# Kernel tuning notes

Measured on AMD Instinct MI355X. Metric: run time of the kernel, lower is better.

## Reference

```python
import jax, jax.numpy as jnp
import numpy as np

B, T, C = 2, 2048, 2048
N_HEADS, N_KV_HEADS = 16, 4
HEAD_DIM = C // N_HEADS  # 128
NUM_GROUPS = N_HEADS // N_KV_HEADS  # 4


def setup_inputs() -> dict:
    key = jax.random.key(0)
    ks = jax.random.split(key, 5)
    s = 1.0 / np.sqrt(C)
    return {
        "x": jax.random.normal(ks[0], (B, T, C), dtype=jnp.float32),
        "Wq": jax.random.normal(ks[1], (C, N_HEADS * HEAD_DIM), dtype=jnp.float32) * s,
        "Wk": jax.random.normal(ks[2], (C, N_KV_HEADS * HEAD_DIM), dtype=jnp.float32) * s,
        "Wv": jax.random.normal(ks[3], (C, N_KV_HEADS * HEAD_DIM), dtype=jnp.float32) * s,
        "Wo": jax.random.normal(ks[4], (C, C), dtype=jnp.float32) * s,
    }


def _rope_tables(seq_len, head_dim, dtype):
    theta = 1.0 / (10000.0 ** (jnp.arange(0, head_dim, 2, dtype=jnp.float32) / head_dim))
    freqs = jnp.arange(seq_len, dtype=jnp.float32)[:, None] * theta[None, :]  # [T, hd/2]
    cos = jnp.concatenate([jnp.cos(freqs), jnp.cos(freqs)], axis=-1)  # [T, hd]
    sin = jnp.concatenate([jnp.sin(freqs), jnp.sin(freqs)], axis=-1)
    return cos.astype(dtype), sin.astype(dtype)


def _rotate_half(x):
    x1, x2 = jnp.split(x, 2, axis=-1)
    return jnp.concatenate([-x2, x1], axis=-1)


def reference(x, Wq, Wk, Wv, Wo):
    b, t, c = x.shape
    q = (x @ Wq).reshape(b, t, N_HEADS, HEAD_DIM).transpose(0, 2, 1, 3)      # [B,H,T,hd]
    k = (x @ Wk).reshape(b, t, N_KV_HEADS, HEAD_DIM).transpose(0, 2, 1, 3)   # [B,Hkv,T,hd]
    v = (x @ Wv).reshape(b, t, N_KV_HEADS, HEAD_DIM).transpose(0, 2, 1, 3)

    cos, sin = _rope_tables(t, HEAD_DIM, x.dtype)  # [T,hd]
    cos = cos[None, None]  # [1,1,T,hd]
    sin = sin[None, None]
    q = q * cos + _rotate_half(q) * sin
    k = k * cos + _rotate_half(k) * sin

    # GQA: expand kv heads (repeat_interleave along head dim)
    k = jnp.repeat(k, NUM_GROUPS, axis=1)  # [B,H,T,hd]
    v = jnp.repeat(v, NUM_GROUPS, axis=1)

    scale = 1.0 / jnp.sqrt(jnp.asarray(HEAD_DIM, dtype=x.dtype))
    scores = jnp.einsum("bhqd,bhkd->bhqk", q, k) * scale  # [B,H,T,T]
    causal = jnp.tril(jnp.ones((t, t), dtype=bool))
    scores = jnp.where(causal[None, None], scores, jnp.asarray(-jnp.inf, dtype=scores.dtype))
    attn = jax.nn.softmax(scores, axis=-1)
    out = jnp.einsum("bhqk,bhkd->bhqd", attn, v)  # [B,H,T,hd]
    out = out.transpose(0, 2, 1, 3).reshape(b, t, c)
    return out @ Wo
```

## Files before the change

kernel.cpp:

```cpp
#include <hip/hip_runtime.h>
#include <hip/hip_bf16.h>
#include <math.h>

typedef __hip_bfloat16 bf16;
typedef __attribute__((ext_vector_type(8))) short bf16x8;
typedef __attribute__((ext_vector_type(4))) float floatx4;

__device__ __forceinline__ void async_copy16(const bf16* g, bf16* l) {
    __builtin_amdgcn_global_load_lds(
        (__attribute__((address_space(1))) void*)(void*)g,
        (__attribute__((address_space(3))) void*)(void*)l,
        16, 0, 0);
}

__global__ __launch_bounds__(256) void cast_f32_bf16(const float* __restrict__ in,
                                                     bf16* __restrict__ out, int n4) {
    int i = blockIdx.x * 256 + threadIdx.x;
    if (i >= n4) return;
    float4 v = ((const float4*)in)[i];
    union { ushort4 u; bf16 b[4]; } o;
    o.b[0] = __float2bfloat16(v.x);
    o.b[1] = __float2bfloat16(v.y);
    o.b[2] = __float2bfloat16(v.z);
    o.b[3] = __float2bfloat16(v.w);
    ((ushort4*)out)[i] = o.u;
}

__global__ __launch_bounds__(256) void cast_transpose(const float* __restrict__ in,
                                                      bf16* __restrict__ out, int K, int N) {
    __shared__ float tile[32][33];
    int nb = blockIdx.x * 32, kb = blockIdx.y * 32;
    for (int j = threadIdx.y; j < 32; j += 8)
        tile[j][threadIdx.x] = in[(size_t)(kb + j) * N + nb + threadIdx.x];
    __syncthreads();
    for (int j = threadIdx.y; j < 32; j += 8)
        out[(size_t)(nb + j) * K + kb + threadIdx.x] = __float2bfloat16(tile[threadIdx.x][j]);
}

template <bool OUTF32>
__global__ __launch_bounds__(256) void gemm_bt(const bf16* __restrict__ A,
                                               const bf16* __restrict__ Bt,
                                               void* __restrict__ Cout,
                                               int M, int N, int K) {
    __shared__ bf16 As[128 * 32];
    __shared__ bf16 Bs[128 * 32];
    const int tid = threadIdx.x;
    const int wave = tid >> 6, lane = tid & 63;
    const int c = lane & 15, quad = lane >> 4;
    const int wm = wave >> 1, wn = wave & 1;
    const int mBase = blockIdx.y * 128, nBase = blockIdx.x * 128;

    const int sRow = lane >> 2;
    const int sCol = ((lane & 3) ^ ((lane >> 3) & 3)) << 3;
    const int rdOff = (quad ^ ((c >> 1) & 3)) << 3;
    const bf16* gA = A + (size_t)(mBase + wave * 32 + sRow) * K + sCol;
    const bf16* gB = Bt + (size_t)(nBase + wave * 32 + sRow) * K + sCol;
    bf16* lA = As + wave * 1024;
    bf16* lB = Bs + wave * 1024;

    floatx4 acc[4][4];
#pragma unroll
    for (int mt = 0; mt < 4; mt++)
#pragma unroll
        for (int nt = 0; nt < 4; nt++) acc[mt][nt] = (floatx4){0.f, 0.f, 0.f, 0.f};

    for (int k0 = 0; k0 < K; k0 += 32) {
        async_copy16(gA + k0, lA);
        async_copy16(gA + k0 + 16 * K, lA + 512);
        async_copy16(gB + k0, lB);
        async_copy16(gB + k0 + 16 * K, lB + 512);
        __syncthreads();
        bf16x8 af[4], bfr[4];
#pragma unroll
        for (int mt = 0; mt < 4; mt++)
            af[mt] = *(const bf16x8*)(As + (wm * 64 + mt * 16 + c) * 32 + rdOff);
#pragma unroll
        for (int nt = 0; nt < 4; nt++)
            bfr[nt] = *(const bf16x8*)(Bs + (wn * 64 + nt * 16 + c) * 32 + rdOff);
#pragma unroll
        for (int mt = 0; mt < 4; mt++)
#pragma unroll
            for (int nt = 0; nt < 4; nt++)
                acc[mt][nt] = __builtin_amdgcn_mfma_f32_16x16x32_bf16(af[mt], bfr[nt],
                                                                      acc[mt][nt], 0, 0, 0);
        __syncthreads();
    }
#pragma unroll
    for (int mt = 0; mt < 4; mt++)
#pragma unroll
        for (int nt = 0; nt < 4; nt++)
#pragma unroll
            for (int r = 0; r < 4; r++) {
                int row = mBase + wm * 64 + mt * 16 + quad * 4 + r;
                int col = nBase + wn * 64 + nt * 16 + c;
                if (OUTF32)
                    ((float*)Cout)[(size_t)row * N + col] = acc[mt][nt][r];
                else
                    ((bf16*)Cout)[(size_t)row * N + col] = __float2bfloat16(acc[mt][nt][r]);
            }
}

__global__ __launch_bounds__(512) void gemm256(const bf16* __restrict__ A,
                                               const bf16* __restrict__ Bt,
                                               bf16* __restrict__ C,
                                               int M, int N, int K) {
    __shared__ bf16 As[4][256 * 32];
    __shared__ bf16 Bs[4][256 * 32];
    const int tid = threadIdx.x;
    const int wave = tid >> 6, lane = tid & 63;
    const int c = lane & 15, quad = lane >> 4;
    const int wm = wave >> 2, wn = wave & 3;
    const int mBase = blockIdx.y * 256, nBase = blockIdx.x * 256;
    const int rdOff = (quad ^ ((c >> 1) & 3)) << 3;

    const bf16* gAs[2];
    const bf16* gBs[2];
#pragma unroll
    for (int i = 0; i < 2; i++) {
        int ci = i * 512 + tid;
        int r = ci >> 2;
        int sc = (ci & 3) ^ ((r >> 1) & 3);
        gAs[i] = A + (size_t)(mBase + r) * K + sc * 8;
        gBs[i] = Bt + (size_t)(nBase + r) * K + sc * 8;
    }
    const int ldsW = wave * 512;

    floatx4 acc[8][4];
#pragma unroll
    for (int mt = 0; mt < 8; mt++)
#pragma unroll
        for (int nt = 0; nt < 4; nt++) acc[mt][nt] = (floatx4){0.f, 0.f, 0.f, 0.f};

    auto stage_half = [&](int t, int i) {
        const int bb = t & 3;
        const int lo = i * 4096 + ldsW;
        async_copy16(gAs[i] + (size_t)t * 32, &As[bb][0] + lo);
        async_copy16(gBs[i] + (size_t)t * 32, &Bs[bb][0] + lo);
    };

    auto tile_body = [&](int t, bool doStage) {
        const int bb = t & 3;
        const bf16* as = &As[bb][0];
        const bf16* bs = &Bs[bb][0];
        bf16x8 bfr[4], af[4];
#pragma unroll
        for (int nt = 0; nt < 4; nt++)
            bfr[nt] = *(const bf16x8*)(bs + (wn * 64 + nt * 16 + c) * 32 + rdOff);
#pragma unroll
        for (int mt = 0; mt < 4; mt++)
            af[mt] = *(const bf16x8*)(as + (wm * 128 + mt * 16 + c) * 32 + rdOff);
        if (doStage) stage_half(t + 2, 0);
        __builtin_amdgcn_s_setprio(1);
#pragma unroll
        for (int mt = 0; mt < 4; mt++)
#pragma unroll
            for (int nt = 0; nt < 4; nt++)
                acc[mt][nt] = __builtin_amdgcn_mfma_f32_16x16x32_bf16(af[mt], bfr[nt],
                                                                      acc[mt][nt], 0, 0, 0);
        __builtin_amdgcn_s_setprio(0);
#pragma unroll
        for (int mt = 0; mt < 4; mt++)
            af[mt] = *(const bf16x8*)(as + (wm * 128 + 64 + mt * 16 + c) * 32 + rdOff);
        if (doStage) stage_half(t + 2, 1);
        __builtin_amdgcn_s_setprio(1);
#pragma unroll
        for (int mt = 0; mt < 4; mt++)
#pragma unroll
            for (int nt = 0; nt < 4; nt++)
                acc[4 + mt][nt] = __builtin_amdgcn_mfma_f32_16x16x32_bf16(af[mt], bfr[nt],
                                                                          acc[4 + mt][nt], 0, 0, 0);
        __builtin_amdgcn_s_setprio(0);
    };

    const int NT = K >> 5;
    stage_half(0, 0); stage_half(0, 1);
    stage_half(1, 0); stage_half(1, 1);
    asm volatile("s_waitcnt vmcnt(4)\n\ts_barrier" ::: "memory");

    for (int t = 0; t < NT - 2; ++t) {
        tile_body(t, true);
        asm volatile("s_waitcnt vmcnt(4)\n\ts_barrier" ::: "memory");
    }
    tile_body(NT - 2, false);
    asm volatile("s_waitcnt vmcnt(0)\n\ts_barrier" ::: "memory");
    tile_body(NT - 1, false);

#pragma unroll
    for (int mt = 0; mt < 8; mt++)
#pragma unroll
        for (int nt = 0; nt < 4; nt++)
#pragma unroll
            for (int r = 0; r < 4; r++) {
                int row = mBase + wm * 128 + mt * 16 + quad * 4 + r;
                int col = nBase + wn * 64 + nt * 16 + c;
                C[(size_t)row * N + col] = __float2bfloat16(acc[mt][nt][r]);
            }
}

__global__ __launch_bounds__(256) void rope_kernel(bf16* __restrict__ X, int heads, int rowStride) {
    int idx = blockIdx.x * 256 + threadIdx.x;
    int d = idx & 63;
    int h = (idx >> 6) % heads;
    int row = idx / (heads * 64);
    int t = row & 2047;
    float theta = exp2f(-(float)d * 0.20762050593045827f);
    float ang = (float)t * theta;
    float sv, cv;
    __sincosf(ang, &sv, &cv);
    bf16* p = X + (size_t)row * rowStride + h * 128 + d;
    float x1 = __bfloat162float(p[0]);
    float x2 = __bfloat162float(p[64]);
    p[0]  = __float2bfloat16(x1 * cv - x2 * sv);
    p[64] = __float2bfloat16(x2 * cv + x1 * sv);
}

__global__ __launch_bounds__(256) void vtrans(const bf16* __restrict__ QKV,
                                              bf16* __restrict__ Vtg) {
    __shared__ bf16 tile[32][34];
    const int bh = blockIdx.z;
    const int b = bh >> 2, kvh = bh & 3;
    const int t0 = blockIdx.x * 32, d0 = blockIdx.y * 32;
    const bf16* src = QKV + (size_t)b * 2048 * 3072 + 2560 + kvh * 128;
    const int tx = threadIdx.x;
    for (int j = threadIdx.y; j < 32; j += 8)
        tile[j][tx] = src[(size_t)(t0 + j) * 3072 + d0 + tx];
    __syncthreads();
    bf16* dst = Vtg + (size_t)bh * 128 * 2048;
    const int g = tx >> 2;
    const int txp = (((g & 3) << 1) | (g >> 2)) * 4 + (tx & 3);
    for (int j = threadIdx.y; j < 32; j += 8)
        dst[(size_t)(d0 + j) * 2048 + t0 + txp] = tile[tx][j];
}

__global__ __launch_bounds__(256, 4) void flash_attn5(const bf16* __restrict__ QKV,
                                                      const bf16* __restrict__ Vtg,
                                                      bf16* __restrict__ Slot0,
                                                      bf16* __restrict__ Slot1,
                                                      float* __restrict__ Ls) {
    const int T = 2048, STR = 3072;
    __shared__ bf16 Ks[4 * 64 * 32];
    __shared__ bf16 Vs[2 * 128 * 32];
    const int b = blockIdx.z, h = blockIdx.y;
    const int pj = blockIdx.x >> 1, s = blockIdx.x & 1;
    const int kvh = h >> 2;
    const int tid = threadIdx.x, wave = tid >> 6, lane = tid & 63;
    const int c = lane & 15, quad = lane >> 4;
    const float C2 = 0.12751541717525597f;

    const bf16* Kg = QKV + (size_t)b * T * STR + 2048 + kvh * 128;
    const bf16* Vg = Vtg + (size_t)(b * 4 + kvh) * 128 * 2048;
    const int srow = tid >> 2;
    const int xcol = ((tid & 3) ^ ((tid >> 3) & 3)) << 3;
    const int koff = (quad ^ ((c >> 1) & 3)) << 3;
    const int qa = 31 - pj;

    auto run_part = [&](int qtile, int ktlo, int kthi, bf16* slot, int lsSlot) {
        const int q0 = qtile * 64;
        bf16x8 qf[4];
        {
            const bf16* qp = QKV + ((size_t)b * T + q0 + wave * 16 + c) * STR + h * 128 + quad * 8;
#pragma unroll
            for (int ks = 0; ks < 4; ks++) qf[ks] = *(const bf16x8*)(qp + ks * 32);
            const float t = (float)(q0 + wave * 16 + c);
#pragma unroll
            for (int ks = 0; ks < 2; ks++)
#pragma unroll
                for (int j = 0; j < 8; j++) {
                    int d = ks * 32 + quad * 8 + j;
                    float theta = exp2f((float)d * -0.20762050593045827f);
                    float sv, cv;
                    __sincosf(t * theta, &sv, &cv);
                    float lo = __bfloat162float(((const bf16*)&qf[ks])[j]);
                    float hi = __bfloat162float(((const bf16*)&qf[ks + 2])[j]);
                    ((bf16*)&qf[ks])[j]     = __float2bfloat16((lo * cv - hi * sv) * C2);
                    ((bf16*)&qf[ks + 2])[j] = __float2bfloat16((hi * cv + lo * sv) * C2);
                }
        }
        floatx4 accO[8];
#pragma unroll
        for (int nt = 0; nt < 8; nt++) accO[nt] = (floatx4){0.f, 0.f, 0.f, 0.f};
        float lsum = 0.f;

        for (int kt = ktlo; kt < kthi; kt++) {
            const int kt0 = kt * 64;
#pragma unroll
            for (int it = 0; it < 4; it++) {
                async_copy16(Kg + (size_t)(kt0 + srow) * STR + it * 32 + xcol,
                             Ks + it * 2048 + wave * 512);
                async_copy16(Vg + (size_t)((it & 1) * 64 + srow) * 2048 + kt0 + (it >> 1) * 32 + xcol,
                             Vs + it * 2048 + wave * 512);
            }
            __syncthreads();
            floatx4 sf[4];
#pragma unroll
            for (int nt = 0; nt < 4; nt++) sf[nt] = (floatx4){0.f, 0.f, 0.f, 0.f};
#pragma unroll
            for (int ks = 0; ks < 4; ks++)
#pragma unroll
                for (int nt = 0; nt < 4; nt++) {
                    bf16x8 kf = *(const bf16x8*)(Ks + ks * 2048 + (nt * 16 + c) * 32 + koff);
                    sf[nt] = __builtin_amdgcn_mfma_f32_16x16x32_bf16(kf, qf[ks], sf[nt], 0, 0, 0);
                }
            if (kt == qtile) {
                const int qrel = wave * 16 + c;
#pragma unroll
                for (int nt = 0; nt < 4; nt++)
#pragma unroll
                    for (int r = 0; r < 4; r++) {
                        float p = exp2f(sf[nt][r]);
                        if (nt * 16 + quad * 4 + r > qrel) p = 0.f;
                        lsum += p;
                        sf[nt][r] = p;
                    }
            } else {
#pragma unroll
                for (int nt = 0; nt < 4; nt++)
#pragma unroll
                    for (int r = 0; r < 4; r++) {
                        float p = exp2f(sf[nt][r]);
                        lsum += p;
                        sf[nt][r] = p;
                    }
            }
#pragma unroll
            for (int kc = 0; kc < 2; kc++) {
                bf16x8 pf;
#pragma unroll
                for (int j = 0; j < 4; j++) {
                    ((bf16*)&pf)[j]     = __float2bfloat16(sf[2 * kc][j]);
                    ((bf16*)&pf)[4 + j] = __float2bfloat16(sf[2 * kc + 1][j]);
                }
#pragma unroll
                for (int nt = 0; nt < 8; nt++) {
                    bf16x8 vf = *(const bf16x8*)(Vs + kc * 4096 + (nt * 16 + c) * 32 + koff);
                    accO[nt] = __builtin_amdgcn_mfma_f32_16x16x32_bf16(pf, vf, accO[nt], 0, 0, 0);
                }
            }
            __syncthreads();
        }
        {
            float v = lsum;
            v += __shfl_xor(v, 16);
            v += __shfl_xor(v, 32);
            if (quad == 0)
                Ls[(size_t)lsSlot * 65536 + ((size_t)(b * 16 + h) * 32 + qtile) * 64
                   + wave * 16 + c] = v;
        }
        const size_t orow = (size_t)b * T + q0 + wave * 16 + quad * 4;
#pragma unroll
        for (int nt = 0; nt < 8; nt++)
#pragma unroll
            for (int r = 0; r < 4; r++)
                slot[(orow + r) * 2048 + h * 128 + nt * 16 + c] =
                    __float2bfloat16(accO[nt][r]);
    };

    if (s == 0) {
        run_part(qa, 0, 17, Slot0, 0);
    } else {
        run_part(qa, 17, 32 - pj, Slot1, 1);
        run_part(pj, 0, pj + 1, Slot0, 0);
    }
}

__global__ __launch_bounds__(256) void attn_merge(bf16* __restrict__ AO,
                                                  const bf16* __restrict__ P1,
                                                  const float* __restrict__ Ls) {
    int i = blockIdx.x * 256 + threadIdx.x;
    int row = i >> 8;
    int cg = (i & 255) << 3;
    int b = row >> 11, t = row & 2047;
    int qtile = t >> 6;
    int h = cg >> 7;
    size_t off = (size_t)row * 2048 + cg;
    size_t li = ((size_t)(b * 16 + h) * 32 + qtile) * 64 + (t & 63);
    bf16x8 a0 = *(const bf16x8*)(AO + off);
    float l = Ls[li];
    float acc[8];
#pragma unroll
    for (int j = 0; j < 8; j++) acc[j] = __bfloat162float(((const bf16*)&a0)[j]);
    if (qtile >= 16) {
        bf16x8 a1 = *(const bf16x8*)(P1 + off);
        l += Ls[65536 + li];
#pragma unroll
        for (int j = 0; j < 8; j++) acc[j] += __bfloat162float(((const bf16*)&a1)[j]);
    }
    float inv = 1.0f / l;
    bf16x8 o;
#pragma unroll
    for (int j = 0; j < 8; j++) ((bf16*)&o)[j] = __float2bfloat16(acc[j] * inv);
    *(bf16x8*)(AO + off) = o;
}

extern "C" void kernel_launch(void* const* d_in, const int* in_sizes, int n_in,
                              void* d_out, int out_size, void* d_ws, size_t ws_size,
                              hipStream_t stream) {
    const float* x  = (const float*)d_in[0];
    const float* Wq = (const float*)d_in[1];
    const float* Wk = (const float*)d_in[2];
    const float* Wv = (const float*)d_in[3];
    const float* Wo = (const float*)d_in[4];

    char* ws = (char*)d_ws;
    bf16* xb   = (bf16*)(ws);
    bf16* Vtg  = (bf16*)(ws);
    bf16* Slt1 = (bf16*)(ws + 4194304);
    float* Ls  = (float*)(ws + 20971520);
    bf16* Wt   = (bf16*)(ws + 16777216);
    bf16* Wot  = (bf16*)(ws + 29360128);
    bf16* QKV  = (bf16*)(ws + 37748736);
    bf16* AO   = (bf16*)(ws + 62914560);

    cast_f32_bf16<<<8192, 256, 0, stream>>>(x, xb, 2097152);
    cast_transpose<<<dim3(64, 64), dim3(32, 8), 0, stream>>>(Wq, Wt, 2048, 2048);
    cast_transpose<<<dim3(16, 64), dim3(32, 8), 0, stream>>>(Wk, Wt + 2048 * 2048, 2048, 512);
    cast_transpose<<<dim3(16, 64), dim3(32, 8), 0, stream>>>(Wv, Wt + 2560 * 2048, 2048, 512);
    cast_transpose<<<dim3(64, 64), dim3(32, 8), 0, stream>>>(Wo, Wot, 2048, 2048);

    gemm256<<<dim3(12, 16), 512, 0, stream>>>(xb, Wt, QKV, 4096, 3072, 2048);

    rope_kernel<<<4096, 256, 0, stream>>>(QKV + 2048, 4, 3072);

    vtrans<<<dim3(64, 4, 8), dim3(32, 8), 0, stream>>>(QKV, Vtg);

    flash_attn5<<<dim3(32, 16, 2), 256, 0, stream>>>(QKV, Vtg, AO, Slt1, Ls);

    attn_merge<<<4096, 256, 0, stream>>>(AO, Slt1, Ls);

    gemm_bt<true><<<dim3(16, 32), 256, 0, stream>>>(AO, Wot, d_out, 4096, 2048, 2048);
}
```

Baseline: 309.4 us.

## Generalize pipelined 512-thread GEMM with templated tiles and block swizzle for both projections

Replaces the simple single-buffered 128x128 output-projection GEMM and the fixed 256x256 QKV GEMM with one templated, 4-stage async-copy pipelined GEMM parameterized by tile size. The QKV projection now uses 256x192 tiles (256 blocks instead of 192, better filling the CUs), and the output projection uses the pipelined kernel with 128x256 tiles instead of the unpipelined one. A block-index remap spreads neighboring blocks across groups for cache/XCD locality. Uneven B-tile loading (some threads issue an extra copy) and per-thread waitcnt counts add complexity and risk of imbalance.

```diff
diff --git a/kernel.cpp b/kernel.cpp
--- a/kernel.cpp
+++ b/kernel.cpp
@@ -11,6 +11,15 @@
         (__attribute__((address_space(1))) void*)(void*)g,
         (__attribute__((address_space(3))) void*)(void*)l,
         16, 0, 0);
+}
+
+template <int N>
+__device__ __forceinline__ void wait_vm_bar() {
+    if constexpr (N == 0) asm volatile("s_waitcnt vmcnt(0)\n\ts_barrier" ::: "memory");
+    else if constexpr (N == 1) asm volatile("s_waitcnt vmcnt(1)\n\ts_barrier" ::: "memory");
+    else if constexpr (N == 2) asm volatile("s_waitcnt vmcnt(2)\n\ts_barrier" ::: "memory");
+    else if constexpr (N == 3) asm volatile("s_waitcnt vmcnt(3)\n\ts_barrier" ::: "memory");
+    else if constexpr (N == 4) asm volatile("s_waitcnt vmcnt(4)\n\ts_barrier" ::: "memory");
 }
 
 __global__ __launch_bounds__(256) void cast_f32_bf16(const float* __restrict__ in,
@@ -37,163 +46,136 @@
         out[(size_t)(nb + j) * K + kb + threadIdx.x] = __float2bfloat16(tile[threadIdx.x][j]);
 }
 
-template <bool OUTF32>
-__global__ __launch_bounds__(256) void gemm_bt(const bf16* __restrict__ A,
-                                               const bf16* __restrict__ Bt,
-                                               void* __restrict__ Cout,
-                                               int M, int N, int K) {
-    __shared__ bf16 As[128 * 32];
-    __shared__ bf16 Bs[128 * 32];
+template <int BM, int BN, bool OUTF32>
+__global__ __launch_bounds__(512) void gemm256g(const bf16* __restrict__ A,
+                                                const bf16* __restrict__ Bt,
+                                                void* __restrict__ Cout,
+                                                int M, int N, int K) {
+    constexpr int CA = BM * 4;
+    constexpr int CB = BN * 4;
+    constexpr int A_LPT = CA / 512;
+    constexpr int EXTRA = CB - 512;
+    constexpr int WM = BM / 2, WN = BN / 4;
+    constexpr int MT = WM / 16, NT = WN / 16;
+    __shared__ bf16 As[4][BM * 32];
+    __shared__ bf16 Bs[4][BN * 32];
     const int tid = threadIdx.x;
     const int wave = tid >> 6, lane = tid & 63;
     const int c = lane & 15, quad = lane >> 4;
-    const int wm = wave >> 1, wn = wave & 1;
-    const int mBase = blockIdx.y * 128, nBase = blockIdx.x * 128;
-
-    const int sRow = lane >> 2;
-    const int sCol = ((lane & 3) ^ ((lane >> 3) & 3)) << 3;
+    const int wm = wave >> 2, wn = wave & 3;
+
+    const int GX = gridDim.x;
+    const int GB = GX * gridDim.y;
+    int bid = blockIdx.y * GX + blockIdx.x;
+    bid = (bid & 7) * (GB >> 3) + (bid >> 3);
+    const int mBase = (bid / GX) * BM, nBase = (bid % GX) * BN;
+
     const int rdOff = (quad ^ ((c >> 1) & 3)) << 3;
-    const bf16* gA = A + (size_t)(mBase + wave * 32 + sRow) * K + sCol;
-    const bf16* gB = Bt + (size_t)(nBase + wave * 32 + sRow) * K + sCol;
-    bf16* lA = As + wave * 1024;
-    bf16* lB = Bs + wave * 1024;
-
-    floatx4 acc[4][4];
-#pragma unroll
-    for (int mt = 0; mt < 4; mt++)
-#pragma unroll
-        for (int nt = 0; nt < 4; nt++) acc[mt][nt] = (floatx4){0.f, 0.f, 0.f, 0.f};
-
-    for (int k0 = 0; k0 < K; k0 += 32) {
-        async_copy16(gA + k0, lA);
-        async_copy16(gA + k0 + 16 * K, lA + 512);
-        async_copy16(gB + k0, lB);
-        async_copy16(gB + k0 + 16 * K, lB + 512);
-        __syncthreads();
-        bf16x8 af[4], bfr[4];
-#pragma unroll
-        for (int mt = 0; mt < 4; mt++)
-            af[mt] = *(const bf16x8*)(As + (wm * 64 + mt * 16 + c) * 32 + rdOff);
-#pragma unroll
-        for (int nt = 0; nt < 4; nt++)
-            bfr[nt] = *(const bf16x8*)(Bs + (wn * 64 + nt * 16 + c) * 32 + rdOff);
-#pragma unroll
-        for (int mt = 0; mt < 4; mt++)
-#pragma unroll
-            for (int nt = 0; nt < 4; nt++)
+    const bool heavy = (EXTRA == 512) ? true : (tid < EXTRA);
+
+    const bf16* gA[A_LPT];
+#pragma unroll
+    for (int s = 0; s < A_LPT; s++) {
+        int ci = s * 512 + tid;
+        int r = ci >> 2;
+        int sc = (ci & 3) ^ ((r >> 1) & 3);
+        gA[s] = A + (size_t)(mBase + r) * K + sc * 8;
+    }
+    const bf16* gB0;
+    {
+        int r = tid >> 2;
+        int sc = (tid & 3) ^ ((r >> 1) & 3);
+        gB0 = Bt + (size_t)(nBase + r) * K + sc * 8;
+    }
+    const bf16* gB1 = nullptr;
+    if (heavy) {
+        int ci = 512 + tid;
+        int r = ci >> 2;
+        int sc = (ci & 3) ^ ((r >> 1) & 3);
+        gB1 = Bt + (size_t)(nBase + r) * K + sc * 8;
+    }
+
+    floatx4 acc[MT][NT];
+#pragma unroll
+    for (int mt = 0; mt < MT; mt++)
+#pragma unroll
+        for (int nt = 0; nt < NT; nt++) acc[mt][nt] = (floatx4){0.f, 0.f, 0.f, 0.f};
+
+    auto stage_a = [&](int t) {
+        const int bb = t & 3;
+#pragma unroll
+        for (int s = 0; s < A_LPT; s++)
+            async_copy16(gA[s] + (size_t)t * 32, &As[bb][(s * 512 + tid) * 8]);
+    };
+    auto stage_b = [&](int t) {
+        const int bb = t & 3;
+        async_copy16(gB0 + (size_t)t * 32, &Bs[bb][tid * 8]);
+        if (heavy) async_copy16(gB1 + (size_t)t * 32, &Bs[bb][(512 + tid) * 8]);
+    };
+    auto boundary = [&]() {
+        if (heavy) wait_vm_bar<A_LPT + 2>();
+        else       wait_vm_bar<A_LPT + 1>();
+    };
+
+    auto tile_body = [&](int t, bool doStage) {
+        const int bb = t & 3;
+        const bf16* as = &As[bb][0];
+        const bf16* bs = &Bs[bb][0];
+        bf16x8 bfr[NT], af[MT / 2];
+#pragma unroll
+        for (int nt = 0; nt < NT; nt++)
+            bfr[nt] = *(const bf16x8*)(bs + (wn * WN + nt * 16 + c) * 32 + rdOff);
+#pragma unroll
+        for (int mt = 0; mt < MT / 2; mt++)
+            af[mt] = *(const bf16x8*)(as + (wm * WM + mt * 16 + c) * 32 + rdOff);
+        if (doStage) stage_a(t + 2);
+        __builtin_amdgcn_s_setprio(1);
+#pragma unroll
+        for (int mt = 0; mt < MT / 2; mt++)
+#pragma unroll
+            for (int nt = 0; nt < NT; nt++)
                 acc[mt][nt] = __builtin_amdgcn_mfma_f32_16x16x32_bf16(af[mt], bfr[nt],
                                                                       acc[mt][nt], 0, 0, 0);
-        __syncthreads();
-    }
-#pragma unroll
-    for (int mt = 0; mt < 4; mt++)
-#pragma unroll
-        for (int nt = 0; nt < 4; nt++)
+        __builtin_amdgcn_s_setprio(0);
+#pragma unroll
+        for (int mt = 0; mt < MT / 2; mt++)
+            af[mt] = *(const bf16x8*)(as + (wm * WM + (MT / 2 + mt) * 16 + c) * 32 + rdOff);
+        if (doStage) stage_b(t + 2);
+        __builtin_amdgcn_s_setprio(1);
+#pragma unroll
+        for (int mt = 0; mt < MT / 2; mt++)
+#pragma unroll
+            for (int nt = 0; nt < NT; nt++)
+                acc[MT / 2 + mt][nt] = __builtin_amdgcn_mfma_f32_16x16x32_bf16(
+                    af[mt], bfr[nt], acc[MT / 2 + mt][nt], 0, 0, 0);
+        __builtin_amdgcn_s_setprio(0);
+    };
+
+    const int NTK = K >> 5;
+    stage_a(0); stage_b(0);
+    stage_a(1); stage_b(1);
+    boundary();
+
+    for (int t = 0; t < NTK - 2; ++t) {
+        tile_body(t, true);
+        boundary();
+    }
+    tile_body(NTK - 2, false);
+    wait_vm_bar<0>();
+    tile_body(NTK - 1, false);
+
+#pragma unroll
+    for (int mt = 0; mt < MT; mt++)
+#pragma unroll
+        for (int nt = 0; nt < NT; nt++)
 #pragma unroll
             for (int r = 0; r < 4; r++) {
-                int row = mBase + wm * 64 + mt * 16 + quad * 4 + r;
-                int col = nBase + wn * 64 + nt * 16 + c;
+                int row = mBase + wm * WM + mt * 16 + quad * 4 + r;
+                int col = nBase + wn * WN + nt * 16 + c;
                 if (OUTF32)
                     ((float*)Cout)[(size_t)row * N + col] = acc[mt][nt][r];
                 else
                     ((bf16*)Cout)[(size_t)row * N + col] = __float2bfloat16(acc[mt][nt][r]);
-            }
-}
-
-__global__ __launch_bounds__(512) void gemm256(const bf16* __restrict__ A,
-                                               const bf16* __restrict__ Bt,
-                                               bf16* __restrict__ C,
-                                               int M, int N, int K) {
-    __shared__ bf16 As[4][256 * 32];
-    __shared__ bf16 Bs[4][256 * 32];
-    const int tid = threadIdx.x;
-    const int wave = tid >> 6, lane = tid & 63;
-    const int c = lane & 15, quad = lane >> 4;
-    const int wm = wave >> 2, wn = wave & 3;
-    const int mBase = blockIdx.y * 256, nBase = blockIdx.x * 256;
-    const int rdOff = (quad ^ ((c >> 1) & 3)) << 3;
-
-    const bf16* gAs[2];
-    const bf16* gBs[2];
-#pragma unroll
-    for (int i = 0; i < 2; i++) {
-        int ci = i * 512 + tid;
-        int r = ci >> 2;
-        int sc = (ci & 3) ^ ((r >> 1) & 3);
-        gAs[i] = A + (size_t)(mBase + r) * K + sc * 8;
-        gBs[i] = Bt + (size_t)(nBase + r) * K + sc * 8;
-    }
-    const int ldsW = wave * 512;
-
-    floatx4 acc[8][4];
-#pragma unroll
-    for (int mt = 0; mt < 8; mt++)
-#pragma unroll
-        for (int nt = 0; nt < 4; nt++) acc[mt][nt] = (floatx4){0.f, 0.f, 0.f, 0.f};
-
-    auto stage_half = [&](int t, int i) {
-        const int bb = t & 3;
-        const int lo = i * 4096 + ldsW;
-        async_copy16(gAs[i] + (size_t)t * 32, &As[bb][0] + lo);
-        async_copy16(gBs[i] + (size_t)t * 32, &Bs[bb][0] + lo);
-    };
-
-    auto tile_body = [&](int t, bool doStage) {
-        const int bb = t & 3;
-        const bf16* as = &As[bb][0];
-        const bf16* bs = &Bs[bb][0];
-        bf16x8 bfr[4], af[4];
-#pragma unroll
-        for (int nt = 0; nt < 4; nt++)
-            bfr[nt] = *(const bf16x8*)(bs + (wn * 64 + nt * 16 + c) * 32 + rdOff);
-#pragma unroll
-        for (int mt = 0; mt < 4; mt++)
-            af[mt] = *(const bf16x8*)(as + (wm * 128 + mt * 16 + c) * 32 + rdOff);
-        if (doStage) stage_half(t + 2, 0);
-        __builtin_amdgcn_s_setprio(1);
-#pragma unroll
-        for (int mt = 0; mt < 4; mt++)
-#pragma unroll
-            for (int nt = 0; nt < 4; nt++)
-                acc[mt][nt] = __builtin_amdgcn_mfma_f32_16x16x32_bf16(af[mt], bfr[nt],
-                                                                      acc[mt][nt], 0, 0, 0);
-        __builtin_amdgcn_s_setprio(0);
-#pragma unroll
-        for (int mt = 0; mt < 4; mt++)
-            af[mt] = *(const bf16x8*)(as + (wm * 128 + 64 + mt * 16 + c) * 32 + rdOff);
-        if (doStage) stage_half(t + 2, 1);
-        __builtin_amdgcn_s_setprio(1);
-#pragma unroll
-        for (int mt = 0; mt < 4; mt++)
-#pragma unroll
-            for (int nt = 0; nt < 4; nt++)
-                acc[4 + mt][nt] = __builtin_amdgcn_mfma_f32_16x16x32_bf16(af[mt], bfr[nt],
-                                                                          acc[4 + mt][nt], 0, 0, 0);
-        __builtin_amdgcn_s_setprio(0);
-    };
-
-    const int NT = K >> 5;
-    stage_half(0, 0); stage_half(0, 1);
-    stage_half(1, 0); stage_half(1, 1);
-    asm volatile("s_waitcnt vmcnt(4)\n\ts_barrier" ::: "memory");
-
-    for (int t = 0; t < NT - 2; ++t) {
-        tile_body(t, true);
-        asm volatile("s_waitcnt vmcnt(4)\n\ts_barrier" ::: "memory");
-    }
-    tile_body(NT - 2, false);
-    asm volatile("s_waitcnt vmcnt(0)\n\ts_barrier" ::: "memory");
-    tile_body(NT - 1, false);
-
-#pragma unroll
-    for (int mt = 0; mt < 8; mt++)
-#pragma unroll
-        for (int nt = 0; nt < 4; nt++)
-#pragma unroll
-            for (int r = 0; r < 4; r++) {
-                int row = mBase + wm * 128 + mt * 16 + quad * 4 + r;
-                int col = nBase + wn * 64 + nt * 16 + c;
-                C[(size_t)row * N + col] = __float2bfloat16(acc[mt][nt][r]);
             }
 }
 
@@ -417,7 +399,7 @@
     cast_transpose<<<dim3(16, 64), dim3(32, 8), 0, stream>>>(Wv, Wt + 2560 * 2048, 2048, 512);
     cast_transpose<<<dim3(64, 64), dim3(32, 8), 0, stream>>>(Wo, Wot, 2048, 2048);
 
-    gemm256<<<dim3(12, 16), 512, 0, stream>>>(xb, Wt, QKV, 4096, 3072, 2048);
+    gemm256g<256, 192, false><<<dim3(16, 16), 512, 0, stream>>>(xb, Wt, QKV, 4096, 3072, 2048);
 
     rope_kernel<<<4096, 256, 0, stream>>>(QKV + 2048, 4, 3072);
 
@@ -427,5 +409,5 @@
 
     attn_merge<<<4096, 256, 0, stream>>>(AO, Slt1, Ls);
 
-    gemm_bt<true><<<dim3(16, 32), 256, 0, stream>>>(AO, Wot, d_out, 4096, 2048, 2048);
-}
+    gemm256g<128, 256, true><<<dim3(8, 32), 512, 0, stream>>>(AO, Wot, d_out, 4096, 2048, 2048);
+}
```

New measurement: 311.9 us. No clear change (+0.8%).
